# Optimization experiments

Hardware: AMD Instinct MI355X
Metric: run time of the kernel (lower is better)

## Reference

```python
import jax, jax.numpy as jnp
import numpy as np

A, N, F, E = 16, 1000, 16, 16000          # agents, nodes/graph, node feat dim, edges/graph
GNN_DIM, RNN_DIM, N_ACT = 128, 128, 16
H1, C1 = 4, 32                             # conv1: 4 heads x 32 ch (concat -> 128)
NEG_SLOPE = 0.2                            # PyG GATv2Conv default


def setup_inputs() -> dict:
    key = jax.random.key(0)
    ks = jax.random.split(key, 16)
    nf = jax.random.normal(ks[0], (A, N, F), dtype=jnp.float32)
    # column 0 is the 'is_self' flag: exactly one agent-node per agent graph
    nf = nf.at[:, :, 0].set(0.0)
    nf = nf.at[jnp.arange(A), jnp.arange(A), 0].set(1.0)
    edge_index = jax.random.randint(ks[1], (2, E), 0, N, dtype=jnp.int32)
    rnn_state = jax.random.normal(ks[2], (A, RNN_DIM), dtype=jnp.float32)
    action_mask = jax.random.randint(ks[3], (A, N_ACT), 0, 2, dtype=jnp.int32)

    def w(k, shape, fan):
        return (jax.random.normal(k, shape, dtype=jnp.float32) / np.sqrt(fan)).astype(jnp.float32)

    params = dict(
        Wl1=w(ks[4], (F, GNN_DIM), F), Wr1=w(ks[5], (F, GNN_DIM), F),
        att1=w(ks[6], (H1, C1), C1), b1=jnp.zeros((GNN_DIM,), jnp.float32),
        ln_w=jnp.ones((GNN_DIM,), jnp.float32), ln_b=jnp.zeros((GNN_DIM,), jnp.float32),
        Wl2=w(ks[7], (GNN_DIM, GNN_DIM), GNN_DIM), Wr2=w(ks[8], (GNN_DIM, GNN_DIM), GNN_DIM),
        att2=w(ks[9], (1, GNN_DIM), GNN_DIM), b2=jnp.zeros((GNN_DIM,), jnp.float32),
        W_ih=w(ks[10], (3 * RNN_DIM, GNN_DIM), GNN_DIM),
        W_hh=w(ks[11], (3 * RNN_DIM, RNN_DIM), RNN_DIM),
        b_ih=jnp.zeros((3 * RNN_DIM,), jnp.float32), b_hh=jnp.zeros((3 * RNN_DIM,), jnp.float32),
        Wa=w(ks[12], (RNN_DIM, N_ACT), RNN_DIM), ba=jnp.zeros((N_ACT,), jnp.float32),
        Wv=w(ks[13], (RNN_DIM, 1), RNN_DIM), bv=jnp.zeros((1,), jnp.float32),
    )
    return dict(node_features=nf, edge_index=edge_index, rnn_state=rnn_state,
                action_mask=action_mask, **params)


def _batched_edges(edge_index):
    # tile edges per agent with node offsets (matches repeat + repeat_interleave order),
    # then add PyG-default self loops
    offsets = (jnp.arange(A, dtype=jnp.int32) * N)  # [A]
    be = (edge_index[:, None, :] + offsets[None, :, None]).reshape(2, A * E)
    loops = jnp.arange(A * N, dtype=jnp.int32)
    src = jnp.concatenate([be[0], loops])
    dst = jnp.concatenate([be[1], loops])
    return src, dst


def _gatv2(x, src, dst, Wl, Wr, att, bias):
    # x: [Nt, Fin]; att: [H, C]
    Hh, C = att.shape
    Nt = x.shape[0]
    xl = (x @ Wl).reshape(Nt, Hh, C)
    xr = (x @ Wr).reshape(Nt, Hh, C)
    e = jnp.einsum('ehc,hc->eh', jax.nn.leaky_relu(xl[src] + xr[dst], NEG_SLOPE), att)  # [Et,H]
    m = jax.ops.segment_max(e, dst, num_segments=Nt)
    a = jnp.exp(e - m[dst])
    s = jax.ops.segment_sum(a, dst, num_segments=Nt)
    alpha = a / s[dst]
    out = jax.ops.segment_sum(alpha[..., None] * xl[src], dst, num_segments=Nt)  # [Nt,H,C]
    return out.reshape(Nt, Hh * C) + bias


def _layer_norm(x, w, b, eps=1e-5):
    mu = jnp.mean(x, axis=-1, keepdims=True)
    var = jnp.mean(jnp.square(x - mu), axis=-1, keepdims=True)
    return (x - mu) * jax.lax.rsqrt(var + eps) * w + b


def _gru_cell(x, h, W_ih, W_hh, b_ih, b_hh):
    gi = x @ W_ih.T + b_ih
    gh = h @ W_hh.T + b_hh
    ir, iz, in_ = jnp.split(gi, 3, axis=-1)
    hr, hz, hn = jnp.split(gh, 3, axis=-1)
    r = jax.nn.sigmoid(ir + hr)
    z = jax.nn.sigmoid(iz + hz)
    n = jnp.tanh(in_ + r * hn)
    return (1.0 - z) * n + z * h


def reference(node_features, edge_index, rnn_state, action_mask,
              Wl1, Wr1, att1, b1, ln_w, ln_b, Wl2, Wr2, att2, b2,
              W_ih, W_hh, b_ih, b_hh, Wa, ba, Wv, bv):
    x = node_features.reshape(-1, F)  # [A*N, F]
    src, dst = _batched_edges(edge_index)
    h = jax.nn.relu(_layer_norm(_gatv2(x, src, dst, Wl1, Wr1, att1, b1), ln_w, ln_b))
    h = _gatv2(h, src, dst, Wl2, Wr2, att2, b2)  # [A*N, 128]
    is_self = node_features[:, :, 0].reshape(-1)
    agent_idx = jnp.nonzero(is_self == 1.0, size=A)[0]
    agent_feat = h[agent_idx]  # [A, 128]
    next_h = _gru_cell(agent_feat, rnn_state, W_ih, W_hh, b_ih, b_hh)
    logits = next_h @ Wa + ba
    logits = jnp.where(action_mask == 0, jnp.float32(-1e8), logits)
    values = next_h @ Wv + bv
    return logits, values, next_h
```

## Files before the change

kernel.cpp:

```cpp
#include <hip/hip_runtime.h>
#include <math.h>

#define A_    16
#define N_    1000
#define F_    16
#define E_    16000
#define D_    128
#define SEG_  8
#define EPB   2000
#define CAPS  16
#define CAP_  48
#define MAXS  49
#define NB_A1 196
#define NB_GH 24

__device__ __forceinline__ float lrelu(float v){ return v > 0.0f ? v : 0.2f*v; }
__device__ __forceinline__ float sigm(float x){ return 1.0f/(1.0f + expf(-x)); }

__device__ __forceinline__ int seg_total(const int* __restrict__ ncnt, int v){
  int t = 0;
  #pragma unroll
  for (int s = 0; s < SEG_; ++s) t += ncnt[v*SEG_ + s];
  return t;
}
__device__ __forceinline__ int seg_lookup(const int* __restrict__ ncnt,
                                          const int* __restrict__ nbrs, int v, int j){
  int base = 0, r = 0;
  bool done = false;
  #pragma unroll
  for (int s = 0; s < SEG_; ++s){
    int c = ncnt[v*SEG_ + s];
    if (!done && j < base + c){ r = nbrs[(v*SEG_ + s)*CAPS + (j - base)]; done = true; }
    base += c;
  }
  return r;
}

__global__ void __launch_bounds__(256) k_pre(
    const int* __restrict__ ei, const float* __restrict__ nf,
    int* __restrict__ ncnt, int* __restrict__ nbrs,
    int* __restrict__ agent_node){
  const int bid = blockIdx.x, tid = threadIdx.x;

  if (bid < SEG_){
    __shared__ int lcnt[N_];
    for (int t = tid; t < N_; t += 256) lcnt[t] = 0;
    __syncthreads();
    const int base = bid*EPB;
    #pragma unroll
    for (int r = 0; r < 8; ++r){
      const int e = base + r*256 + tid;
      if (e < base + EPB && e < E_){
        int src = ei[e], dst = ei[E_ + e];
        int pos = atomicAdd(&lcnt[dst], 1);
        if (pos < CAPS) nbrs[(dst*SEG_ + bid)*CAPS + pos] = src;
      }
    }
    __syncthreads();
    for (int t = tid; t < N_; t += 256) ncnt[t*SEG_ + bid] = min(lcnt[t], CAPS);
  } else {
    const int a = bid - SEG_;
    for (int t = tid; t < N_; t += 256)
      if (nf[(size_t)(a*N_ + t)*F_] == 1.0f) agent_node[a] = t;
  }
}

__global__ void __launch_bounds__(256) k_mid(
    const float* __restrict__ nf, const int* __restrict__ agent_node,
    const int* __restrict__ ncnt, const int* __restrict__ nbrs,
    const float* __restrict__ Wl1, const float* __restrict__ Wr1,
    const float* __restrict__ att1, const float* __restrict__ b1,
    const float* __restrict__ lnw, const float* __restrict__ lnb,
    const float* __restrict__ Wl2, const float* __restrict__ Wr2,
    const float* __restrict__ hs, const float* __restrict__ Whh,
    const float* __restrict__ bhh,
    float* __restrict__ xl2_c, float* __restrict__ xr2g,
    float* __restrict__ ghb){
  const int tid  = threadIdx.x;

  if (blockIdx.x >= NB_A1){
    const int rg = (blockIdx.x - NB_A1)*256 + tid;
    const int a = rg/384, r = rg - a*384;
    const float4* w4 = (const float4*)&Whh[r*D_];
    const float4* x4 = (const float4*)&hs[a*D_];
    float acc = bhh[r];
    #pragma unroll
    for (int k = 0; k < D_/4; ++k){
      float4 w = w4[k], x = x4[k];
      acc += w.x*x.x + w.y*x.y + w.z*x.z + w.w*x.w;
    }
    ghb[a*384 + r] = acc;
    return;
  }

  const int lane = tid & 63;
  const int wv   = tid >> 6;
  const int wid  = blockIdx.x*4 + wv;
  const int a = wid / MAXS;
  const int i = wid - a*MAXS;
  const int d_a  = agent_node[a];
  const int dega = min(seg_total(ncnt, d_a), CAP_);
  if (i > dega) return;
  const int v   = (i == 0) ? d_a : seg_lookup(ncnt, nbrs, d_a, i-1);
  const int deg = min(seg_total(ncnt, v), CAP_);
  const int c0  = lane*2;

  __shared__ float feat[4][MAXS*F_];
  float* fb = feat[wv];

  int nid = (lane < deg) ? seg_lookup(ncnt, nbrs, v, lane) : 0;
  for (int t = lane; t < (deg+1)*4; t += 64){
    int j = t >> 2, q = (t & 3)*4;
    int s = (j == 0) ? v : __shfl(nid, j-1);
    *(float4*)&fb[j*F_ + q] = *(const float4*)&nf[((size_t)a*N_ + s)*F_ + q];
  }
  asm volatile("s_waitcnt lgkmcnt(0)" ::: "memory");

  float wl0[F_], wl1c[F_];
  #pragma unroll
  for (int k = 0; k < F_; ++k){
    float2 w = *(const float2*)&Wl1[k*D_ + c0];
    wl0[k] = w.x; wl1c[k] = w.y;
  }
  float xr0 = 0.f, xr1 = 0.f;
  #pragma unroll
  for (int k = 0; k < F_; ++k){
    float2 w = *(const float2*)&Wr1[k*D_ + c0];
    float xv = fb[k];
    xr0 += xv*w.x; xr1 += xv*w.y;
  }
  const int head = lane >> 4;
  const float at0 = att1[head*32 + (c0 & 31)];
  const float at1 = att1[head*32 + ((c0+1) & 31)];

  float m = -INFINITY, ls = 0.f, ac0 = 0.f, ac1 = 0.f;
  for (int j = 0; j <= deg; ++j){
    const float* fr = &fb[j*F_];
    float xl0 = 0.f, xl1 = 0.f;
    #pragma unroll
    for (int k = 0; k < F_; k += 4){
      float4 xv = *(const float4*)&fr[k];
      xl0 += xv.x*wl0[k]  + xv.y*wl0[k+1]  + xv.z*wl0[k+2]  + xv.w*wl0[k+3];
      xl1 += xv.x*wl1c[k] + xv.y*wl1c[k+1] + xv.z*wl1c[k+2] + xv.w*wl1c[k+3];
    }
    float t = lrelu(xl0 + xr0)*at0 + lrelu(xl1 + xr1)*at1;
    t += __shfl_xor(t,1); t += __shfl_xor(t,2);
    t += __shfl_xor(t,4); t += __shfl_xor(t,8);
    float mn = fmaxf(m, t);
    float sc = expf(m - mn), p = expf(t - mn);
    ls = ls*sc + p; ac0 = ac0*sc + p*xl0; ac1 = ac1*sc + p*xl1;
    m = mn;
  }
  float inv = 1.0f/ls;
  float v0 = ac0*inv + b1[c0], v1 = ac1*inv + b1[c0+1];
  float ss = v0 + v1;
  ss += __shfl_xor(ss,1); ss += __shfl_xor(ss,2); ss += __shfl_xor(ss,4);
  ss += __shfl_xor(ss,8); ss += __shfl_xor(ss,16); ss += __shfl_xor(ss,32);
  float mu = ss*(1.0f/D_);
  float d0 = v0 - mu, d1 = v1 - mu;
  float vs = d0*d0 + d1*d1;
  vs += __shfl_xor(vs,1); vs += __shfl_xor(vs,2); vs += __shfl_xor(vs,4);
  vs += __shfl_xor(vs,8); vs += __shfl_xor(vs,16); vs += __shfl_xor(vs,32);
  float rinv = rsqrtf(vs*(1.0f/D_) + 1e-5f);
  float h0 = fmaxf(d0*rinv*lnw[c0]   + lnb[c0],   0.0f);
  float h1 = fmaxf(d1*rinv*lnw[c0+1] + lnb[c0+1], 0.0f);

  fb[c0] = h0; fb[c0+1] = h1;
  asm volatile("s_waitcnt lgkmcnt(0)" ::: "memory");

  float xa0 = 0.f, xa1 = 0.f;
  #pragma unroll 8
  for (int k = 0; k < D_; k += 4){
    float4 hv = *(const float4*)&fb[k];
    float2 w0 = *(const float2*)&Wl2[(k+0)*D_ + c0];
    float2 w1 = *(const float2*)&Wl2[(k+1)*D_ + c0];
    float2 w2 = *(const float2*)&Wl2[(k+2)*D_ + c0];
    float2 w3 = *(const float2*)&Wl2[(k+3)*D_ + c0];
    xa0 += hv.x*w0.x + hv.y*w1.x + hv.z*w2.x + hv.w*w3.x;
    xa1 += hv.x*w0.y + hv.y*w1.y + hv.z*w2.y + hv.w*w3.y;
  }
  *(float2*)&xl2_c[((size_t)a*MAXS + i)*D_ + c0] = make_float2(xa0, xa1);

  if (i == 0){
    float xb0 = 0.f, xb1 = 0.f;
    #pragma unroll 8
    for (int k = 0; k < D_; k += 4){
      float4 hv = *(const float4*)&fb[k];
      float2 w0 = *(const float2*)&Wr2[(k+0)*D_ + c0];
      float2 w1 = *(const float2*)&Wr2[(k+1)*D_ + c0];
      float2 w2 = *(const float2*)&Wr2[(k+2)*D_ + c0];
      float2 w3 = *(const float2*)&Wr2[(k+3)*D_ + c0];
      xb0 += hv.x*w0.x + hv.y*w1.x + hv.z*w2.x + hv.w*w3.x;
      xb1 += hv.x*w0.y + hv.y*w1.y + hv.z*w2.y + hv.w*w3.y;
    }
    *(float2*)&xr2g[a*D_ + c0] = make_float2(xb0, xb1);
  }
}

__global__ void __launch_bounds__(1024) k_tail(
    const float* __restrict__ xl2_c, const float* __restrict__ xr2g,
    const float* __restrict__ ghb,
    const int* __restrict__ agent_node, const int* __restrict__ ncnt,
    const float* __restrict__ hs, const int* __restrict__ am,
    const float* __restrict__ att2, const float* __restrict__ b2,
    const float* __restrict__ Wih, const float* __restrict__ bih,
    const float* __restrict__ Wa, const float* __restrict__ ba,
    const float* __restrict__ Wv, const float* __restrict__ bv,
    float* __restrict__ out){
  const int a    = blockIdx.x;
  const int tid  = threadIdx.x;
  const int lane = tid & 63;
  const int wv   = tid >> 6;

  __shared__ float xsl[MAXS][D_];
  __shared__ float xr2s[D_], afl[D_], ghl[3*D_], gbuf[3*D_], hsrow[D_], nh[D_];
  __shared__ float scores[64];

  const int d_a = agent_node[a];
  const int ns  = min(seg_total(ncnt, d_a), CAP_) + 1;

  for (int t = tid; t < ns*(D_/4); t += 1024){
    int j = t >> 5, q = t & 31;
    ((float4*)xsl[j])[q] = ((const float4*)&xl2_c[((size_t)a*MAXS + j)*D_])[q];
  }
  if (tid < D_) hsrow[tid] = hs[a*D_ + tid];
  else if (tid < 4*D_) ghl[tid - D_] = ghb[a*384 + (tid - D_)];
  else if (tid < 5*D_) xr2s[tid - 4*D_] = xr2g[a*D_ + (tid - 4*D_)];
  __syncthreads();

  {
    const int c0 = lane*2;
    const float xr0 = xr2s[c0], xr1 = xr2s[c0+1];
    const float at0 = att2[c0], at1 = att2[c0+1];
    for (int q = 0; q < 4; ++q){
      const int s = wv + q*16;
      if (s < ns){
        float2 xl = *(const float2*)&xsl[s][c0];
        float t = lrelu(xl.x + xr0)*at0 + lrelu(xl.y + xr1)*at1;
        t += __shfl_xor(t,1);  t += __shfl_xor(t,2);  t += __shfl_xor(t,4);
        t += __shfl_xor(t,8);  t += __shfl_xor(t,16); t += __shfl_xor(t,32);
        if (lane == 0) scores[s] = t;
      }
    }
  }
  __syncthreads();
  if (wv == 0){
    float sc = (lane < ns) ? scores[lane] : -INFINITY;
    float m = sc;
    m = fmaxf(m, __shfl_xor(m,1));  m = fmaxf(m, __shfl_xor(m,2));
    m = fmaxf(m, __shfl_xor(m,4));  m = fmaxf(m, __shfl_xor(m,8));
    m = fmaxf(m, __shfl_xor(m,16)); m = fmaxf(m, __shfl_xor(m,32));
    float p = (lane < ns) ? expf(sc - m) : 0.f;
    float s = p;
    s += __shfl_xor(s,1);  s += __shfl_xor(s,2);  s += __shfl_xor(s,4);
    s += __shfl_xor(s,8);  s += __shfl_xor(s,16); s += __shfl_xor(s,32);
    if (lane < ns) scores[lane] = p/s;
  }
  __syncthreads();
  if (tid < D_){
    float acc = 0.f;
    for (int i = 0; i < ns; ++i) acc += scores[i]*xsl[i][tid];
    afl[tid] = acc + b2[tid];
  }
  __syncthreads();

  #pragma unroll
  for (int p = 0; p < 3; ++p){
    const int r  = p*128 + (tid >> 3);
    const int kk = (tid & 7)*16;
    const float4* w4 = (const float4*)&Wih[r*D_ + kk];
    float acc = 0.f;
    #pragma unroll
    for (int q = 0; q < 4; ++q){
      float4 w = w4[q];
      float4 x = *(const float4*)&afl[kk + q*4];
      acc += w.x*x.x + w.y*x.y + w.z*x.z + w.w*x.w;
    }
    acc += __shfl_xor(acc,1); acc += __shfl_xor(acc,2); acc += __shfl_xor(acc,4);
    if ((tid & 7) == 0) gbuf[r] = acc + bih[r];
  }
  __syncthreads();

  if (tid < D_){
    float r = sigm(gbuf[tid]         + ghl[tid]);
    float z = sigm(gbuf[D_ + tid]    + ghl[D_ + tid]);
    float n = tanhf(gbuf[2*D_ + tid] + r*ghl[2*D_ + tid]);
    float nv = (1.0f - z)*n + z*hsrow[tid];
    nh[tid] = nv;
    out[272 + a*D_ + tid] = nv;
  }
  __syncthreads();

  if (wv == 0){
    const int j = lane & 15, q = lane >> 4;
    float acc = 0.f;
    #pragma unroll 8
    for (int k = q*32; k < q*32 + 32; ++k) acc += nh[k]*Wa[k*16 + j];
    acc += __shfl_xor(acc,16); acc += __shfl_xor(acc,32);
    if (lane < 16){
      float lg = acc + ba[j];
      if (am[a*16 + j] == 0) lg = -1e8f;
      out[a*16 + j] = lg;
    }
  } else if (wv == 1){
    const int c0 = lane*2;
    float acc = nh[c0]*Wv[c0] + nh[c0+1]*Wv[c0+1];
    acc += __shfl_xor(acc,1);  acc += __shfl_xor(acc,2);  acc += __shfl_xor(acc,4);
    acc += __shfl_xor(acc,8);  acc += __shfl_xor(acc,16); acc += __shfl_xor(acc,32);
    if (lane == 0) out[256 + a] = acc + bv[0];
  }
}

extern "C" void kernel_launch(void* const* d_in, const int* in_sizes, int n_in,
                              void* d_out, int out_size, void* d_ws, size_t ws_size,
                              hipStream_t stream){
  const float* nf   = (const float*)d_in[0];
  const int*   ei   = (const int*)  d_in[1];
  const float* hs   = (const float*)d_in[2];
  const int*   am   = (const int*)  d_in[3];
  const float* Wl1  = (const float*)d_in[4];
  const float* Wr1  = (const float*)d_in[5];
  const float* att1 = (const float*)d_in[6];
  const float* b1   = (const float*)d_in[7];
  const float* lnw  = (const float*)d_in[8];
  const float* lnb  = (const float*)d_in[9];
  const float* Wl2  = (const float*)d_in[10];
  const float* Wr2  = (const float*)d_in[11];
  const float* att2 = (const float*)d_in[12];
  const float* b2   = (const float*)d_in[13];
  const float* Wih  = (const float*)d_in[14];
  const float* Whh  = (const float*)d_in[15];
  const float* bih  = (const float*)d_in[16];
  const float* bhh  = (const float*)d_in[17];
  const float* Wa   = (const float*)d_in[18];
  const float* ba   = (const float*)d_in[19];
  const float* Wv   = (const float*)d_in[20];
  const float* bv   = (const float*)d_in[21];
  float* out = (float*)d_out;

  int* wsI = (int*)d_ws;
  int*   ncnt       = wsI;
  int*   agent_node = wsI + 8000;
  int*   nbrs       = wsI + 8192;
  float* xl2_c      = (float*)(wsI + 136192);
  float* xr2g       = (float*)(wsI + 236544);
  float* ghb        = (float*)(wsI + 238592);

  k_pre <<<SEG_ + A_, 256, 0, stream>>>(ei, nf, ncnt, nbrs, agent_node);
  k_mid <<<NB_A1 + NB_GH, 256, 0, stream>>>(nf, agent_node, ncnt, nbrs,
                                            Wl1, Wr1, att1, b1, lnw, lnb,
                                            Wl2, Wr2, hs, Whh, bhh,
                                            xl2_c, xr2g, ghb);
  k_tail<<<A_, 1024, 0, stream>>>(xl2_c, xr2g, ghb, agent_node, ncnt, hs, am,
                                  att2, b2, Wih, bih, Wa, ba, Wv, bv, out);
}
```

Measured before the change: 33.88 us.

## Drop preprocessing kernel; each block rescans edges to find needed neighbours

```diff
diff --git a/kernel.cpp b/kernel.cpp
--- a/kernel.cpp
+++ b/kernel.cpp
@@ -6,68 +6,17 @@
 #define F_    16
 #define E_    16000
 #define D_    128
-#define SEG_  8
-#define EPB   2000
-#define CAPS  16
 #define CAP_  48
 #define MAXS  49
 #define NB_A1 196
 #define NB_GH 24
+#define CHK   63
 
 __device__ __forceinline__ float lrelu(float v){ return v > 0.0f ? v : 0.2f*v; }
 __device__ __forceinline__ float sigm(float x){ return 1.0f/(1.0f + expf(-x)); }
 
-__device__ __forceinline__ int seg_total(const int* __restrict__ ncnt, int v){
-  int t = 0;
-  #pragma unroll
-  for (int s = 0; s < SEG_; ++s) t += ncnt[v*SEG_ + s];
-  return t;
-}
-__device__ __forceinline__ int seg_lookup(const int* __restrict__ ncnt,
-                                          const int* __restrict__ nbrs, int v, int j){
-  int base = 0, r = 0;
-  bool done = false;
-  #pragma unroll
-  for (int s = 0; s < SEG_; ++s){
-    int c = ncnt[v*SEG_ + s];
-    if (!done && j < base + c){ r = nbrs[(v*SEG_ + s)*CAPS + (j - base)]; done = true; }
-    base += c;
-  }
-  return r;
-}
-
-__global__ void __launch_bounds__(256) k_pre(
-    const int* __restrict__ ei, const float* __restrict__ nf,
-    int* __restrict__ ncnt, int* __restrict__ nbrs,
-    int* __restrict__ agent_node){
-  const int bid = blockIdx.x, tid = threadIdx.x;
-
-  if (bid < SEG_){
-    __shared__ int lcnt[N_];
-    for (int t = tid; t < N_; t += 256) lcnt[t] = 0;
-    __syncthreads();
-    const int base = bid*EPB;
-    #pragma unroll
-    for (int r = 0; r < 8; ++r){
-      const int e = base + r*256 + tid;
-      if (e < base + EPB && e < E_){
-        int src = ei[e], dst = ei[E_ + e];
-        int pos = atomicAdd(&lcnt[dst], 1);
-        if (pos < CAPS) nbrs[(dst*SEG_ + bid)*CAPS + pos] = src;
-      }
-    }
-    __syncthreads();
-    for (int t = tid; t < N_; t += 256) ncnt[t*SEG_ + bid] = min(lcnt[t], CAPS);
-  } else {
-    const int a = bid - SEG_;
-    for (int t = tid; t < N_; t += 256)
-      if (nf[(size_t)(a*N_ + t)*F_] == 1.0f) agent_node[a] = t;
-  }
-}
-
 __global__ void __launch_bounds__(256) k_mid(
-    const float* __restrict__ nf, const int* __restrict__ agent_node,
-    const int* __restrict__ ncnt, const int* __restrict__ nbrs,
+    const float* __restrict__ nf, const int* __restrict__ ei,
     const float* __restrict__ Wl1, const float* __restrict__ Wr1,
     const float* __restrict__ att1, const float* __restrict__ b1,
     const float* __restrict__ lnw, const float* __restrict__ lnb,
@@ -76,7 +25,7 @@
     const float* __restrict__ bhh,
     float* __restrict__ xl2_c, float* __restrict__ xr2g,
     float* __restrict__ ghb){
-  const int tid  = threadIdx.x;
+  const int tid = threadIdx.x;
 
   if (blockIdx.x >= NB_A1){
     const int rg = (blockIdx.x - NB_A1)*256 + tid;
@@ -93,25 +42,105 @@
     return;
   }
 
+  const int bid  = blockIdx.x;
   const int lane = tid & 63;
   const int wv   = tid >> 6;
-  const int wid  = blockIdx.x*4 + wv;
-  const int a = wid / MAXS;
-  const int i = wid - a*MAXS;
-  const int d_a  = agent_node[a];
-  const int dega = min(seg_total(ncnt, d_a), CAP_);
-  if (i > dega) return;
-  const int v   = (i == 0) ? d_a : seg_lookup(ncnt, nbrs, d_a, i-1);
-  const int deg = min(seg_total(ncnt, v), CAP_);
+  const int wid  = bid*4 + wv;
+  const int a_w  = wid / MAXS;
+  const int i_w  = wid - a_w*MAXS;
+  const int a0   = (bid*4) / MAXS;
+  const int a1   = (bid*4 + 3) / MAXS;
+  const int nag  = (a1 > a0) ? 2 : 1;
+
+  __shared__ float feat[4][MAXS*F_];
+  __shared__ int   sslot[2][MAXS];
+  __shared__ int   nbrw[4][CAP_];
+  __shared__ int   sh_da[2];
+  __shared__ int   pc[2][4];
+  __shared__ int   vnode[4];
+  __shared__ int   ncw[4];
+
+  for (int g = 0; g < nag; ++g){
+    const int ag = a0 + g;
+    for (int t = tid; t < N_; t += 256)
+      if (nf[(size_t)(ag*N_ + t)*F_] == 1.0f) sh_da[g] = t;
+  }
+  if (tid < 4) ncw[tid] = 0;
+  __syncthreads();
+
+  const int e0 = tid*CHK;
+  int cnt[2] = {0, 0};
+  for (int q = 0; q < CHK; ++q){
+    const int e = e0 + q;
+    if (e >= E_) break;
+    const int dst = ei[E_ + e];
+    if (dst == sh_da[0]) cnt[0]++;
+    if (nag > 1 && dst == sh_da[1]) cnt[1]++;
+  }
+  int pre[2];
+  #pragma unroll
+  for (int g = 0; g < 2; ++g){
+    int x = cnt[g];
+    #pragma unroll
+    for (int off = 1; off < 64; off <<= 1){
+      int y = __shfl_up(x, off);
+      if (lane >= off) x += y;
+    }
+    if (lane == 63) pc[g][wv] = x;
+    pre[g] = x - cnt[g];
+  }
+  __syncthreads();
+  int degA[2];
+  #pragma unroll
+  for (int g = 0; g < 2; ++g){
+    int base = 0, tot = 0;
+    #pragma unroll
+    for (int w2 = 0; w2 < 4; ++w2){ if (w2 < wv) base += pc[g][w2]; tot += pc[g][w2]; }
+    pre[g] += base; degA[g] = tot;
+  }
+
+  {
+    int o0 = pre[0], o1 = pre[1];
+    for (int q = 0; q < CHK; ++q){
+      const int e = e0 + q;
+      if (e >= E_) break;
+      const int dst = ei[E_ + e];
+      if (dst == sh_da[0]){ if (o0 < MAXS-1) sslot[0][1 + o0] = ei[e]; o0++; }
+      if (nag > 1 && dst == sh_da[1]){ if (o1 < MAXS-1) sslot[1][1 + o1] = ei[e]; o1++; }
+    }
+  }
+  if (tid < nag) sslot[tid][0] = sh_da[tid];
+  __syncthreads();
+
+  const int g_w  = a_w - a0;
+  const int dega = min(degA[g_w], MAXS-1);
+  const bool active = (i_w <= dega);
+  const int v = active ? sslot[g_w][i_w] : -1;
+  if (lane == 0) vnode[wv] = v;
+  __syncthreads();
+
+  for (int q = 0; q < CHK; ++q){
+    const int e = e0 + q;
+    if (e >= E_) break;
+    const int dst = ei[E_ + e];
+    #pragma unroll
+    for (int w2 = 0; w2 < 4; ++w2){
+      if (dst == vnode[w2]){
+        int pos = atomicAdd(&ncw[w2], 1);
+        if (pos < CAP_) nbrw[w2][pos] = ei[e];
+      }
+    }
+  }
+  __syncthreads();
+  if (!active) return;
+  const int a   = a_w;
+  const int deg = min(ncw[wv], CAP_);
   const int c0  = lane*2;
-
-  __shared__ float feat[4][MAXS*F_];
   float* fb = feat[wv];
 
-  int nid = (lane < deg) ? seg_lookup(ncnt, nbrs, v, lane) : 0;
   for (int t = lane; t < (deg+1)*4; t += 64){
     int j = t >> 2, q = (t & 3)*4;
-    int s = (j == 0) ? v : __shfl(nid, j-1);
+    int s = (j == 0) ? v : nbrw[wv][j-1];
     *(float4*)&fb[j*F_ + q] = *(const float4*)&nf[((size_t)a*N_ + s)*F_ + q];
   }
   asm volatile("s_waitcnt lgkmcnt(0)" ::: "memory");
@@ -179,9 +208,9 @@
     xa0 += hv.x*w0.x + hv.y*w1.x + hv.z*w2.x + hv.w*w3.x;
     xa1 += hv.x*w0.y + hv.y*w1.y + hv.z*w2.y + hv.w*w3.y;
   }
-  *(float2*)&xl2_c[((size_t)a*MAXS + i)*D_ + c0] = make_float2(xa0, xa1);
-
-  if (i == 0){
+  *(float2*)&xl2_c[((size_t)a*MAXS + i_w)*D_ + c0] = make_float2(xa0, xa1);
+
+  if (i_w == 0){
     float xb0 = 0.f, xb1 = 0.f;
     #pragma unroll 8
     for (int k = 0; k < D_; k += 4){
@@ -200,7 +229,7 @@
 __global__ void __launch_bounds__(1024) k_tail(
     const float* __restrict__ xl2_c, const float* __restrict__ xr2g,
     const float* __restrict__ ghb,
-    const int* __restrict__ agent_node, const int* __restrict__ ncnt,
+    const float* __restrict__ nf, const int* __restrict__ ei,
     const float* __restrict__ hs, const int* __restrict__ am,
     const float* __restrict__ att2, const float* __restrict__ b2,
     const float* __restrict__ Wih, const float* __restrict__ bih,
@@ -215,17 +244,32 @@
   __shared__ float xsl[MAXS][D_];
   __shared__ float xr2s[D_], afl[D_], ghl[3*D_], gbuf[3*D_], hsrow[D_], nh[D_];
   __shared__ float scores[64];
-
-  const int d_a = agent_node[a];
-  const int ns  = min(seg_total(ncnt, d_a), CAP_) + 1;
-
+  __shared__ int   sh_da, sh_cnt;
+
+  if (tid == 0) sh_cnt = 0;
+  if (tid < N_ && nf[(size_t)(a*N_ + tid)*F_] == 1.0f) sh_da = tid;
+  __syncthreads();
+  const int d_a = sh_da;
+  {
+    int c = 0;
+    #pragma unroll
+    for (int q = 0; q < 16; ++q){
+      const int e = q*1024 + tid;
+      if (e < E_ && ei[E_ + e] == d_a) c++;
+    }
+    c += __shfl_xor(c,1);  c += __shfl_xor(c,2);  c += __shfl_xor(c,4);
+    c += __shfl_xor(c,8);  c += __shfl_xor(c,16); c += __shfl_xor(c,32);
+    if (lane == 0 && c) atomicAdd(&sh_cnt, c);
+  }
+  if (tid < D_) hsrow[tid] = hs[a*D_ + tid];
+  else if (tid < 4*D_) ghl[tid - D_] = ghb[a*384 + (tid - D_)];
+  else if (tid < 5*D_) xr2s[tid - 4*D_] = xr2g[a*D_ + (tid - 4*D_)];
+  __syncthreads();
+  const int ns = min(sh_cnt, CAP_) + 1;
   for (int t = tid; t < ns*(D_/4); t += 1024){
     int j = t >> 5, q = t & 31;
     ((float4*)xsl[j])[q] = ((const float4*)&xl2_c[((size_t)a*MAXS + j)*D_])[q];
   }
-  if (tid < D_) hsrow[tid] = hs[a*D_ + tid];
-  else if (tid < 4*D_) ghl[tid - D_] = ghb[a*384 + (tid - D_)];
-  else if (tid < 5*D_) xr2s[tid - 4*D_] = xr2g[a*D_ + (tid - 4*D_)];
   __syncthreads();
 
   {
@@ -338,19 +382,14 @@
   const float* bv   = (const float*)d_in[21];
   float* out = (float*)d_out;
 
-  int* wsI = (int*)d_ws;
-  int*   ncnt       = wsI;
-  int*   agent_node = wsI + 8000;
-  int*   nbrs       = wsI + 8192;
-  float* xl2_c      = (float*)(wsI + 136192);
-  float* xr2g       = (float*)(wsI + 236544);
-  float* ghb        = (float*)(wsI + 238592);
-
-  k_pre <<<SEG_ + A_, 256, 0, stream>>>(ei, nf, ncnt, nbrs, agent_node);
-  k_mid <<<NB_A1 + NB_GH, 256, 0, stream>>>(nf, agent_node, ncnt, nbrs,
-                                            Wl1, Wr1, att1, b1, lnw, lnb,
+  float* wsF = (float*)d_ws;
+  float* xl2_c = wsF;
+  float* xr2g  = wsF + 100352;
+  float* ghb   = wsF + 102400;
+
+  k_mid <<<NB_A1 + NB_GH, 256, 0, stream>>>(nf, ei, Wl1, Wr1, att1, b1, lnw, lnb,
                                             Wl2, Wr2, hs, Whh, bhh,
                                             xl2_c, xr2g, ghb);
-  k_tail<<<A_, 1024, 0, stream>>>(xl2_c, xr2g, ghb, agent_node, ncnt, hs, am,
+  k_tail<<<A_, 1024, 0, stream>>>(xl2_c, xr2g, ghb, nf, ei, hs, am,
                                   att2, b2, Wih, bih, Wa, ba, Wv, bv, out);
 }
```

Result: slower. 71.91 us (+112.3%).
